# Kernel tuning notes

Hardware: AMD Instinct MI355X
Metric: run time of the kernel (lower is better)

Reference implementation:

```python
import jax, jax.numpy as jnp
import numpy as np

# Hard-coded video-latent geometry from the module's tile/untile rearranges
NT, NH, NW = 6, 6, 6          # tile grid
TT, TH, TW = 6, 8, 8          # tile sizes (6*8*8 = 384 tokens per tile)
TILE = TT * TH * TW           # 384
NTILES = NT * NH * NW         # 216
SEQ = NTILES * TILE           # 82944 = 36*48*48
# per-head sliding-tile windows (w_t, w_h, w_w), i.e. mask_strategy (sp_size=1)
WINDOWS = ((2, 1, 1), (1, 2, 2), (1, 1, 2), (1, 1, 1))


def tile(x):
    # 'b (t h w) head d' with (t,h,w)=(36,48,48) ->
    # 'b (n_t n_h n_w ts_t ts_h ts_w) head d'  (sp_size = 1)
    b, s, H, d = x.shape
    x = x.reshape(b, NT, TT, NH, TH, NW, TW, H, d)
    x = x.transpose(0, 1, 3, 5, 2, 4, 6, 7, 8)  # b, nt, nh, nw, tst, tsh, tsw, H, d
    return x.reshape(b, s, H, d)


def untile(x):
    b, s, H, d = x.shape
    x = x.reshape(b, NT, NH, NW, TT, TH, TW, H, d)
    x = x.transpose(0, 1, 4, 2, 5, 3, 6, 7, 8)  # b, nt, tst, nh, tsh, nw, tsw, H, d
    return x.reshape(b, s, H, d)


def _axis_window(w, n):
    # allowed key tile indices per query tile along one axis, clamped at borders
    q = jnp.arange(n)
    start = jnp.clip(q - (w - 1) // 2, 0, n - w)
    return start[:, None] + jnp.arange(w)[None, :]  # [n, w]


def _tile_gather_idx(wt, wh, ww):
    # flat key-tile ids [NTILES, wt*wh*ww] for every query tile
    it = _axis_window(wt, NT)  # [NT, wt]
    ih = _axis_window(wh, NH)  # [NH, wh]
    iw = _axis_window(ww, NW)  # [NW, ww]
    idx = (it[:, None, None, :, None, None] * (NH * NW)
           + ih[None, :, None, None, :, None] * NW
           + iw[None, None, :, None, None, :])
    return idx.reshape(NTILES, wt * wh * ww)


def sliding_tile_attention(q, k, v):
    # q, k, v: [B, S, H, d] in TILED order; returns [B, S, H, d] tiled order
    B, S, H, d = q.shape
    scale = 1.0 / jnp.sqrt(jnp.asarray(d, q.dtype))
    qt = q.reshape(B, NTILES, TILE, H, d)
    kt = k.reshape(B, NTILES, TILE, H, d)
    vt = v.reshape(B, NTILES, TILE, H, d)
    outs = []
    for h, (wt, wh, ww) in enumerate(WINDOWS):
        idx = _tile_gather_idx(wt, wh, ww)            # [NTILES, W]
        qh = qt[:, :, :, h, :]                        # [B, Q, 384, d]
        kg = kt[:, :, :, h, :][:, idx]                # [B, Q, W, 384, d]
        vg = vt[:, :, :, h, :][:, idx]
        W = idx.shape[1]
        kg = kg.reshape(B, NTILES, W * TILE, d)
        vg = vg.reshape(B, NTILES, W * TILE, d)
        s = jnp.einsum('bqnd,bqmd->bqnm', qh, kg) * scale
        p = jax.nn.softmax(s, axis=-1)
        outs.append(jnp.einsum('bqnm,bqmd->bqnd', p, vg))
    o = jnp.stack(outs, axis=3)                       # [B, Q, 384, H, d]
    return o.reshape(B, S, H, d)


def setup_inputs() -> dict:
    key = jax.random.key(0)
    kq, kk, kv = jax.random.split(key, 3)
    B, H, d = 1, 4, 64
    q = jax.random.normal(kq, (B, SEQ, H, d), dtype=jnp.float32)
    k = jax.random.normal(kk, (B, SEQ, H, d), dtype=jnp.float32)
    v = jax.random.normal(kv, (B, SEQ, H, d), dtype=jnp.float32)
    return {'q': q, 'k': k, 'v': v}


def reference(q, k, v):
    # parallel_attn_func, STA branch, sp_size = 1 (no sequence parallelism)
    qt_, kt_, vt_ = tile(q), tile(k), tile(v)
    x = sliding_tile_attention(qt_, kt_, vt_)
    return untile(x)
```

## Files before the change

### kernel.cpp

```cpp
#include <hip/hip_runtime.h>

typedef _Float16 half4 __attribute__((ext_vector_type(4)));
typedef _Float16 half8 __attribute__((ext_vector_type(8)));
typedef float    f32x4 __attribute__((ext_vector_type(4)));
typedef unsigned int u32x2 __attribute__((ext_vector_type(2)));
typedef unsigned int u32x4 __attribute__((ext_vector_type(4)));

__device__ __forceinline__ unsigned int pkrtz(float a, float b) {
    return __builtin_bit_cast(unsigned int, __builtin_amdgcn_cvt_pkrtz(a, b));
}
__device__ __forceinline__ half4 pack4(float a, float b, float c, float d) {
    u32x2 t; t[0] = pkrtz(a, b); t[1] = pkrtz(c, d);
    return __builtin_bit_cast(half4, t);
}
__device__ __forceinline__ half8 pack8(float a, float b, float c, float d,
                                       float e, float f, float gg, float h) {
    u32x4 t; t[0] = pkrtz(a, b); t[1] = pkrtz(c, d);
    t[2] = pkrtz(e, f); t[3] = pkrtz(gg, h);
    return __builtin_bit_cast(half8, t);
}
__device__ __forceinline__ float fexp2(float x) {
    return __builtin_amdgcn_exp2f(x);
}

#define ROWF 256
#define HDIM 64

__device__ __forceinline__ int intra_off(int j) {
    return 2304 * (j >> 6) + 48 * ((j >> 3) & 7) + (j & 7);
}

__device__ __forceinline__ int kperm32(int x) {
    return ((x & 4) << 2) | ((x & 24) >> 1) | (x & 3);
}

__global__ __launch_bounds__(512) void sta_kernel(
    const float* __restrict__ qg, const float* __restrict__ kg,
    const float* __restrict__ vg, float* __restrict__ out)
{
    __shared__ _Float16 Klds[128 * 64];
    __shared__ _Float16 Vlds[64 * 128];

    const int tid  = threadIdx.x;
    const int wave = tid >> 6;
    const int lane = tid & 63;
    const int g    = lane >> 4;
    const int c    = lane & 15;
    const int csw  = c >> 1;

    const int bid  = blockIdx.x;
    const int hidx = bid / 216;
    const int tile = bid - hidx * 216;
    const int head = (hidx == 0) ? 1 : (hidx == 1 ? 0 : hidx);

    const int nt = tile / 36;
    const int nh = (tile / 6) % 6;
    const int nw = tile % 6;
    const int tbase = 13824 * nt + 384 * nh + 8 * nw;

    int W, kb0; unsigned long long dpk;
    const int t0 = nt < 4 ? nt : 4;
    const int h0 = nh < 4 ? nh : 4;
    const int w0 = nw < 4 ? nw : 4;
    if (head == 0) {
        W = 2; kb0 = 13824 * t0 + 384 * nh + 8 * nw; dpk = (13824ULL << 16);
    } else if (head == 1) {
        W = 4; kb0 = 13824 * nt + 384 * h0 + 8 * w0;
        dpk = (8ULL << 16) | (384ULL << 32) | (392ULL << 48);
    } else if (head == 2) {
        W = 2; kb0 = 13824 * nt + 384 * nh + 8 * w0; dpk = (8ULL << 16);
    } else {
        W = 1; kb0 = tbase; dpk = 0ULL;
    }
    const int NC = W * 3;

    const float qscale = 0.125f * 1.44269504f;
    half8 qf[3][2];
    #pragma unroll
    for (int mt = 0; mt < 3; ++mt) {
        const int j = wave * 48 + mt * 16 + c;
        const float* qp = qg + (size_t)(tbase + intra_off(j)) * ROWF + head * HDIM;
        #pragma unroll
        for (int kc = 0; kc < 2; ++kc) {
            f32x4 a = *(const f32x4*)(qp + kc * 32 + g * 8);
            f32x4 b = *(const f32x4*)(qp + kc * 32 + g * 8 + 4);
            qf[mt][kc] = pack8(a[0] * qscale, a[1] * qscale, a[2] * qscale, a[3] * qscale,
                               b[0] * qscale, b[1] * qscale, b[2] * qscale, b[3] * qscale);
        }
    }

    f32x4 oacc[3][4];
    float m_r[3], l_r[3];
    #pragma unroll
    for (int mt = 0; mt < 3; ++mt) {
        #pragma unroll
        for (int dt = 0; dt < 4; ++dt) oacc[mt][dt] = (f32x4){0.f, 0.f, 0.f, 0.f};
        m_r[mt] = 8.0f;
        l_r[mt] = 0.f;
    }

    const int r4  = tid >> 4;
    const int sc4 = tid & 15;

    int toff0, toff1, toff2, toff3, krow0;
    {
        const int r0 = r4 * 4;
        toff0 = intra_off(r0 + 0);
        toff1 = intra_off(r0 + 1);
        toff2 = intra_off(r0 + 2);
        toff3 = intra_off(r0 + 3);
        krow0 = (r0 & 96) + kperm32(r0 & 31);
    }
    const size_t lin = (size_t)head * HDIM + sc4 * 4;

    f32x4 kr0, kr1, kr2, kr3, vr0, vr1, vr2, vr3;

#define ISSUE_N(N) do {                                                  \
        const int wi_ = (N) / 3;                                         \
        const int kb_ = kb0 + (int)((dpk >> (wi_ * 16)) & 0xFFFFULL)     \
                            + 4608 * ((N) - wi_ * 3);                    \
        const size_t a0 = (size_t)(kb_ + toff0) * ROWF + lin;            \
        const size_t a1 = (size_t)(kb_ + toff1) * ROWF + lin;            \
        const size_t a2 = (size_t)(kb_ + toff2) * ROWF + lin;            \
        const size_t a3 = (size_t)(kb_ + toff3) * ROWF + lin;            \
        kr0 = *(const f32x4*)(kg + a0); vr0 = *(const f32x4*)(vg + a0);  \
        kr1 = *(const f32x4*)(kg + a1); vr1 = *(const f32x4*)(vg + a1);  \
        kr2 = *(const f32x4*)(kg + a2); vr2 = *(const f32x4*)(vg + a2);  \
        kr3 = *(const f32x4*)(kg + a3); vr3 = *(const f32x4*)(vg + a3);  \
    } while (0)

#define COMMIT() do {                                                        \
        _Pragma("unroll")                                                    \
        for (int j = 0; j < 4; ++j) {                                        \
            const int kr_ = krow0 + j;                                       \
            const int ko_ = kr_ * 64 +                                       \
                (((sc4 >> 1) ^ ((kr_ >> 1) & 7)) << 3) + ((sc4 & 1) << 2);   \
            const f32x4 kv = (j == 0) ? kr0 : (j == 1) ? kr1                 \
                             : (j == 2) ? kr2 : kr3;                         \
            *(half4*)&Klds[ko_] = pack4(kv[0], kv[1], kv[2], kv[3]);         \
        }                                                                    \
        _Pragma("unroll")                                                    \
        for (int e = 0; e < 4; ++e) {                                        \
            const int vr_ = sc4 * 4 + e;                                     \
            const int vo_ = vr_ * 128 +                                      \
                (((r4 >> 1) ^ ((vr_ >> 1) & 7)) << 3) + ((r4 & 1) << 2);     \
            *(half4*)&Vlds[vo_] = pack4(vr0[e], vr1[e], vr2[e], vr3[e]);     \
        }                                                                    \
    } while (0)

    ISSUE_N(0);

    for (int ci = 0; ci < NC; ++ci) {
        COMMIT();
        __syncthreads();
        if (ci + 1 < NC) ISSUE_N(ci + 1);

        #pragma unroll
        for (int s = 0; s < 4; ++s) {
            f32x4 sacc[3][2];
            #pragma unroll
            for (int mt = 0; mt < 3; ++mt) {
                const float nm = -m_r[mt];
                sacc[mt][0] = (f32x4){nm, nm, nm, nm};
                sacc[mt][1] = (f32x4){nm, nm, nm, nm};
            }
            #pragma unroll
            for (int kc = 0; kc < 2; ++kc) {
                #pragma unroll
                for (int jt = 0; jt < 2; ++jt) {
                    const half8 kf = *(const half8*)
                        &Klds[(s * 32 + jt * 16 + c) * 64 + (((kc * 4 + g) ^ csw) << 3)];
                    #pragma unroll
                    for (int mt = 0; mt < 3; ++mt)
                        sacc[mt][jt] = __builtin_amdgcn_mfma_f32_16x16x32_f16(
                            kf, qf[mt][kc], sacc[mt][jt], 0, 0, 0);
                }
            }

            half8 pa[3];
            #pragma unroll
            for (int mt = 0; mt < 3; ++mt) {
                float p0 = fexp2(sacc[mt][0][0]), p1 = fexp2(sacc[mt][0][1]);
                float p2 = fexp2(sacc[mt][0][2]), p3 = fexp2(sacc[mt][0][3]);
                float p4 = fexp2(sacc[mt][1][0]), p5 = fexp2(sacc[mt][1][1]);
                float p6 = fexp2(sacc[mt][1][2]), p7 = fexp2(sacc[mt][1][3]);
                const float ma = fmaxf(fmaxf(fmaxf(sacc[mt][0][0], sacc[mt][0][1]),
                                             sacc[mt][0][2]), sacc[mt][0][3]);
                const float mb = fmaxf(fmaxf(fmaxf(sacc[mt][1][0], sacc[mt][1][1]),
                                             sacc[mt][1][2]), sacc[mt][1][3]);
                const float mm = fmaxf(ma, mb);

                if (__builtin_expect(!__all(mm <= 12.f), 0)) {
                    float mrow = mm;
                    mrow = fmaxf(mrow, __shfl_xor(mrow, 16, 64));
                    mrow = fmaxf(mrow, __shfl_xor(mrow, 32, 64));
                    const float delta = fmaxf(mrow, 0.f);
                    const float alpha = fexp2(-delta);
                    m_r[mt] += delta;
                    l_r[mt] *= alpha;
                    p0 *= alpha; p1 *= alpha; p2 *= alpha; p3 *= alpha;
                    p4 *= alpha; p5 *= alpha; p6 *= alpha; p7 *= alpha;
                    float ar[4];
                    #pragma unroll
                    for (int r = 0; r < 4; ++r) ar[r] = __shfl(alpha, g * 4 + r, 16);
                    #pragma unroll
                    for (int r = 0; r < 4; ++r)
                        #pragma unroll
                        for (int dt = 0; dt < 4; ++dt)
                            oacc[mt][dt][r] *= ar[r];
                }

                l_r[mt] += ((p0 + p1) + (p2 + p3)) + ((p4 + p5) + (p6 + p7));
                pa[mt] = pack8(p0, p1, p2, p3, p4, p5, p6, p7);
            }

            #pragma unroll
            for (int dt = 0; dt < 4; ++dt) {
                const half8 vb = *(const half8*)
                    &Vlds[(dt * 16 + c) * 128 + ((((s << 2) | g) ^ csw) << 3)];
                #pragma unroll
                for (int mt = 0; mt < 3; ++mt)
                    oacc[mt][dt] = __builtin_amdgcn_mfma_f32_16x16x32_f16(
                        pa[mt], vb, oacc[mt][dt], 0, 0, 0);
            }
        }
        __syncthreads();
    }
#undef ISSUE_N
#undef COMMIT

    #pragma unroll
    for (int mt = 0; mt < 3; ++mt) {
        float lf = l_r[mt];
        lf += __shfl_xor(lf, 16, 64);
        lf += __shfl_xor(lf, 32, 64);
        float lq[4];
        #pragma unroll
        for (int r = 0; r < 4; ++r) lq[r] = __shfl(lf, g * 4 + r, 16);
        #pragma unroll
        for (int r = 0; r < 4; ++r) {
            const int j = wave * 48 + mt * 16 + g * 4 + r;
            float* op = out + (size_t)(tbase + intra_off(j)) * ROWF + head * HDIM;
            const float linv = __builtin_amdgcn_rcpf(lq[r]);
            #pragma unroll
            for (int dt = 0; dt < 4; ++dt)
                op[dt * 16 + c] = oacc[mt][dt][r] * linv;
        }
    }
}

extern "C" void kernel_launch(void* const* d_in, const int* in_sizes, int n_in,
                              void* d_out, int out_size, void* d_ws, size_t ws_size,
                              hipStream_t stream) {
    const float* q = (const float*)d_in[0];
    const float* k = (const float*)d_in[1];
    const float* v = (const float*)d_in[2];
    float* o = (float*)d_out;
    dim3 grid(216 * 4);
    dim3 block(512);
    hipLaunchKernelGGL(sta_kernel, grid, block, 0, stream, q, k, v, o);
}
```

Baseline: 132.6 us.

## Compute softmax row sums via MFMA with ones and interleave heads per tile

```diff
diff --git a/kernel.cpp b/kernel.cpp
--- a/kernel.cpp
+++ b/kernel.cpp
@@ -49,9 +49,8 @@
     const int csw  = c >> 1;
 
     const int bid  = blockIdx.x;
-    const int hidx = bid / 216;
-    const int tile = bid - hidx * 216;
-    const int head = (hidx == 0) ? 1 : (hidx == 1 ? 0 : hidx);
+    const int tile = bid >> 2;
+    const int head = (bid + tile) & 3;
 
     const int nt = tile / 36;
     const int nh = (tile / 6) % 6;
@@ -89,14 +88,18 @@
         }
     }
 
+    u32x4 onep; onep[0] = onep[1] = onep[2] = onep[3] = 0x3C003C00u;
+    const half8 ones8 = __builtin_bit_cast(half8, onep);
+
     f32x4 oacc[3][4];
-    float m_r[3], l_r[3];
+    f32x4 lacc[3];
+    float m_r[3];
     #pragma unroll
     for (int mt = 0; mt < 3; ++mt) {
         #pragma unroll
         for (int dt = 0; dt < 4; ++dt) oacc[mt][dt] = (f32x4){0.f, 0.f, 0.f, 0.f};
+        lacc[mt] = (f32x4){0.f, 0.f, 0.f, 0.f};
         m_r[mt] = 8.0f;
-        l_r[mt] = 0.f;
     }
 
     const int r4  = tid >> 4;
@@ -184,10 +187,10 @@
                 float p2 = fexp2(sacc[mt][0][2]), p3 = fexp2(sacc[mt][0][3]);
                 float p4 = fexp2(sacc[mt][1][0]), p5 = fexp2(sacc[mt][1][1]);
                 float p6 = fexp2(sacc[mt][1][2]), p7 = fexp2(sacc[mt][1][3]);
-                const float ma = fmaxf(fmaxf(fmaxf(sacc[mt][0][0], sacc[mt][0][1]),
-                                             sacc[mt][0][2]), sacc[mt][0][3]);
-                const float mb = fmaxf(fmaxf(fmaxf(sacc[mt][1][0], sacc[mt][1][1]),
-                                             sacc[mt][1][2]), sacc[mt][1][3]);
+                const float ma = fmaxf(fmaxf(sacc[mt][0][0], sacc[mt][0][1]),
+                                       fmaxf(sacc[mt][0][2], sacc[mt][0][3]));
+                const float mb = fmaxf(fmaxf(sacc[mt][1][0], sacc[mt][1][1]),
+                                       fmaxf(sacc[mt][1][2], sacc[mt][1][3]));
                 const float mm = fmaxf(ma, mb);
 
                 if (__builtin_expect(!__all(mm <= 12.f), 0)) {
@@ -197,23 +200,27 @@
                     const float delta = fmaxf(mrow, 0.f);
                     const float alpha = fexp2(-delta);
                     m_r[mt] += delta;
-                    l_r[mt] *= alpha;
                     p0 *= alpha; p1 *= alpha; p2 *= alpha; p3 *= alpha;
                     p4 *= alpha; p5 *= alpha; p6 *= alpha; p7 *= alpha;
                     float ar[4];
                     #pragma unroll
                     for (int r = 0; r < 4; ++r) ar[r] = __shfl(alpha, g * 4 + r, 16);
                     #pragma unroll
-                    for (int r = 0; r < 4; ++r)
+                    for (int r = 0; r < 4; ++r) {
+                        lacc[mt][r] *= ar[r];
                         #pragma unroll
                         for (int dt = 0; dt < 4; ++dt)
                             oacc[mt][dt][r] *= ar[r];
+                    }
                 }
 
-                l_r[mt] += ((p0 + p1) + (p2 + p3)) + ((p4 + p5) + (p6 + p7));
                 pa[mt] = pack8(p0, p1, p2, p3, p4, p5, p6, p7);
             }
 
+            #pragma unroll
+            for (int mt = 0; mt < 3; ++mt)
+                lacc[mt] = __builtin_amdgcn_mfma_f32_16x16x32_f16(
+                    pa[mt], ones8, lacc[mt], 0, 0, 0);
             #pragma unroll
             for (int dt = 0; dt < 4; ++dt) {
                 const half8 vb = *(const half8*)
@@ -231,17 +238,11 @@
 
     #pragma unroll
     for (int mt = 0; mt < 3; ++mt) {
-        float lf = l_r[mt];
-        lf += __shfl_xor(lf, 16, 64);
-        lf += __shfl_xor(lf, 32, 64);
-        float lq[4];
-        #pragma unroll
-        for (int r = 0; r < 4; ++r) lq[r] = __shfl(lf, g * 4 + r, 16);
         #pragma unroll
         for (int r = 0; r < 4; ++r) {
             const int j = wave * 48 + mt * 16 + g * 4 + r;
             float* op = out + (size_t)(tbase + intra_off(j)) * ROWF + head * HDIM;
-            const float linv = __builtin_amdgcn_rcpf(lq[r]);
+            const float linv = __builtin_amdgcn_rcpf(lacc[mt][r]);
             #pragma unroll
             for (int dt = 0; dt < 4; ++dt)
                 op[dt * 16 + c] = oacc[mt][dt][r] * linv;
```

After: 212.1 us. 60.0% more time.

## Use persistent blocks with atomic work-stealing queue over tile-head items

Applied to the files above, without the earlier changes.

```diff
diff --git a/kernel.cpp b/kernel.cpp
--- a/kernel.cpp
+++ b/kernel.cpp
@@ -25,6 +25,7 @@
 
 #define ROWF 256
 #define HDIM 64
+#define NWORK 864
 
 __device__ __forceinline__ int intra_off(int j) {
     return 2304 * (j >> 6) + 48 * ((j >> 3) & 7) + (j & 7);
@@ -36,10 +37,12 @@
 
 __global__ __launch_bounds__(512) void sta_kernel(
     const float* __restrict__ qg, const float* __restrict__ kg,
-    const float* __restrict__ vg, float* __restrict__ out)
+    const float* __restrict__ vg, float* __restrict__ out,
+    int* __restrict__ wcnt)
 {
     __shared__ _Float16 Klds[128 * 64];
     __shared__ _Float16 Vlds[64 * 128];
+    __shared__ int s_w;
 
     const int tid  = threadIdx.x;
     const int wave = tid >> 6;
@@ -47,57 +50,6 @@
     const int g    = lane >> 4;
     const int c    = lane & 15;
     const int csw  = c >> 1;
-
-    const int bid  = blockIdx.x;
-    const int hidx = bid / 216;
-    const int tile = bid - hidx * 216;
-    const int head = (hidx == 0) ? 1 : (hidx == 1 ? 0 : hidx);
-
-    const int nt = tile / 36;
-    const int nh = (tile / 6) % 6;
-    const int nw = tile % 6;
-    const int tbase = 13824 * nt + 384 * nh + 8 * nw;
-
-    int W, kb0; unsigned long long dpk;
-    const int t0 = nt < 4 ? nt : 4;
-    const int h0 = nh < 4 ? nh : 4;
-    const int w0 = nw < 4 ? nw : 4;
-    if (head == 0) {
-        W = 2; kb0 = 13824 * t0 + 384 * nh + 8 * nw; dpk = (13824ULL << 16);
-    } else if (head == 1) {
-        W = 4; kb0 = 13824 * nt + 384 * h0 + 8 * w0;
-        dpk = (8ULL << 16) | (384ULL << 32) | (392ULL << 48);
-    } else if (head == 2) {
-        W = 2; kb0 = 13824 * nt + 384 * nh + 8 * w0; dpk = (8ULL << 16);
-    } else {
-        W = 1; kb0 = tbase; dpk = 0ULL;
-    }
-    const int NC = W * 3;
-
-    const float qscale = 0.125f * 1.44269504f;
-    half8 qf[3][2];
-    #pragma unroll
-    for (int mt = 0; mt < 3; ++mt) {
-        const int j = wave * 48 + mt * 16 + c;
-        const float* qp = qg + (size_t)(tbase + intra_off(j)) * ROWF + head * HDIM;
-        #pragma unroll
-        for (int kc = 0; kc < 2; ++kc) {
-            f32x4 a = *(const f32x4*)(qp + kc * 32 + g * 8);
-            f32x4 b = *(const f32x4*)(qp + kc * 32 + g * 8 + 4);
-            qf[mt][kc] = pack8(a[0] * qscale, a[1] * qscale, a[2] * qscale, a[3] * qscale,
-                               b[0] * qscale, b[1] * qscale, b[2] * qscale, b[3] * qscale);
-        }
-    }
-
-    f32x4 oacc[3][4];
-    float m_r[3], l_r[3];
-    #pragma unroll
-    for (int mt = 0; mt < 3; ++mt) {
-        #pragma unroll
-        for (int dt = 0; dt < 4; ++dt) oacc[mt][dt] = (f32x4){0.f, 0.f, 0.f, 0.f};
-        m_r[mt] = 8.0f;
-        l_r[mt] = 0.f;
-    }
 
     const int r4  = tid >> 4;
     const int sc4 = tid & 15;
@@ -111,9 +63,67 @@
         toff3 = intra_off(r0 + 3);
         krow0 = (r0 & 96) + kperm32(r0 & 31);
     }
-    const size_t lin = (size_t)head * HDIM + sc4 * 4;
+    const float qscale = 0.125f * 1.44269504f;
 
     f32x4 kr0, kr1, kr2, kr3, vr0, vr1, vr2, vr3;
+
+    for (;;) {
+        __syncthreads();
+        if (tid == 0) s_w = atomicAdd(wcnt, 1);
+        __syncthreads();
+        const int w = s_w;
+        if (w >= NWORK) return;
+
+        const int hidx = w / 216;
+        const int tile = w - hidx * 216;
+        const int head = (hidx == 0) ? 1 : (hidx == 1 ? 0 : hidx);
+
+        const int nt = tile / 36;
+        const int nh = (tile / 6) % 6;
+        const int nw = tile % 6;
+        const int tbase = 13824 * nt + 384 * nh + 8 * nw;
+
+        int W, kb0; unsigned long long dpk;
+        const int t0 = nt < 4 ? nt : 4;
+        const int h0 = nh < 4 ? nh : 4;
+        const int w0 = nw < 4 ? nw : 4;
+        if (head == 0) {
+            W = 2; kb0 = 13824 * t0 + 384 * nh + 8 * nw; dpk = (13824ULL << 16);
+        } else if (head == 1) {
+            W = 4; kb0 = 13824 * nt + 384 * h0 + 8 * w0;
+            dpk = (8ULL << 16) | (384ULL << 32) | (392ULL << 48);
+        } else if (head == 2) {
+            W = 2; kb0 = 13824 * nt + 384 * nh + 8 * w0; dpk = (8ULL << 16);
+        } else {
+            W = 1; kb0 = tbase; dpk = 0ULL;
+        }
+        const int NC = W * 3;
+
+        half8 qf[3][2];
+        #pragma unroll
+        for (int mt = 0; mt < 3; ++mt) {
+            const int j = wave * 48 + mt * 16 + c;
+            const float* qp = qg + (size_t)(tbase + intra_off(j)) * ROWF + head * HDIM;
+            #pragma unroll
+            for (int kc = 0; kc < 2; ++kc) {
+                f32x4 a = *(const f32x4*)(qp + kc * 32 + g * 8);
+                f32x4 b = *(const f32x4*)(qp + kc * 32 + g * 8 + 4);
+                qf[mt][kc] = pack8(a[0] * qscale, a[1] * qscale, a[2] * qscale, a[3] * qscale,
+                                   b[0] * qscale, b[1] * qscale, b[2] * qscale, b[3] * qscale);
+            }
+        }
+
+        f32x4 oacc[3][4];
+        float m_r[3], l_r[3];
+        #pragma unroll
+        for (int mt = 0; mt < 3; ++mt) {
+            #pragma unroll
+            for (int dt = 0; dt < 4; ++dt) oacc[mt][dt] = (f32x4){0.f, 0.f, 0.f, 0.f};
+            m_r[mt] = 8.0f;
+            l_r[mt] = 0.f;
+        }
+
+        const size_t lin = (size_t)head * HDIM + sc4 * 4;
 
 #define ISSUE_N(N) do {                                                  \
         const int wi_ = (N) / 3;                                         \
@@ -148,103 +158,104 @@
         }                                                                    \
     } while (0)
 
-    ISSUE_N(0);
-
-    for (int ci = 0; ci < NC; ++ci) {
-        COMMIT();
-        __syncthreads();
-        if (ci + 1 < NC) ISSUE_N(ci + 1);
-
-        #pragma unroll
-        for (int s = 0; s < 4; ++s) {
-            f32x4 sacc[3][2];
-            #pragma unroll
-            for (int mt = 0; mt < 3; ++mt) {
-                const float nm = -m_r[mt];
-                sacc[mt][0] = (f32x4){nm, nm, nm, nm};
-                sacc[mt][1] = (f32x4){nm, nm, nm, nm};
-            }
-            #pragma unroll
-            for (int kc = 0; kc < 2; ++kc) {
-                #pragma unroll
-                for (int jt = 0; jt < 2; ++jt) {
-                    const half8 kf = *(const half8*)
-                        &Klds[(s * 32 + jt * 16 + c) * 64 + (((kc * 4 + g) ^ csw) << 3)];
+        ISSUE_N(0);
+
+        for (int ci = 0; ci < NC; ++ci) {
+            COMMIT();
+            __syncthreads();
+            if (ci + 1 < NC) ISSUE_N(ci + 1);
+
+            #pragma unroll
+            for (int s = 0; s < 4; ++s) {
+                f32x4 sacc[3][2];
+                #pragma unroll
+                for (int mt = 0; mt < 3; ++mt) {
+                    const float nm = -m_r[mt];
+                    sacc[mt][0] = (f32x4){nm, nm, nm, nm};
+                    sacc[mt][1] = (f32x4){nm, nm, nm, nm};
+                }
+                #pragma unroll
+                for (int kc = 0; kc < 2; ++kc) {
+                    #pragma unroll
+                    for (int jt = 0; jt < 2; ++jt) {
+                        const half8 kf = *(const half8*)
+                            &Klds[(s * 32 + jt * 16 + c) * 64 + (((kc * 4 + g) ^ csw) << 3)];
+                        #pragma unroll
+                        for (int mt = 0; mt < 3; ++mt)
+                            sacc[mt][jt] = __builtin_amdgcn_mfma_f32_16x16x32_f16(
+                                kf, qf[mt][kc], sacc[mt][jt], 0, 0, 0);
+                    }
+                }
+
+                half8 pa[3];
+                #pragma unroll
+                for (int mt = 0; mt < 3; ++mt) {
+                    float p0 = fexp2(sacc[mt][0][0]), p1 = fexp2(sacc[mt][0][1]);
+                    float p2 = fexp2(sacc[mt][0][2]), p3 = fexp2(sacc[mt][0][3]);
+                    float p4 = fexp2(sacc[mt][1][0]), p5 = fexp2(sacc[mt][1][1]);
+                    float p6 = fexp2(sacc[mt][1][2]), p7 = fexp2(sacc[mt][1][3]);
+                    const float ma = fmaxf(fmaxf(sacc[mt][0][0], sacc[mt][0][1]),
+                                           fmaxf(sacc[mt][0][2], sacc[mt][0][3]));
+                    const float mb = fmaxf(fmaxf(sacc[mt][1][0], sacc[mt][1][1]),
+                                           fmaxf(sacc[mt][1][2], sacc[mt][1][3]));
+                    const float mm = fmaxf(ma, mb);
+
+                    if (__builtin_expect(!__all(mm <= 12.f), 0)) {
+                        float mrow = mm;
+                        mrow = fmaxf(mrow, __shfl_xor(mrow, 16, 64));
+                        mrow = fmaxf(mrow, __shfl_xor(mrow, 32, 64));
+                        const float delta = fmaxf(mrow, 0.f);
+                        const float alpha = fexp2(-delta);
+                        m_r[mt] += delta;
+                        l_r[mt] *= alpha;
+                        p0 *= alpha; p1 *= alpha; p2 *= alpha; p3 *= alpha;
+                        p4 *= alpha; p5 *= alpha; p6 *= alpha; p7 *= alpha;
+                        float ar[4];
+                        #pragma unroll
+                        for (int r = 0; r < 4; ++r) ar[r] = __shfl(alpha, g * 4 + r, 16);
+                        #pragma unroll
+                        for (int r = 0; r < 4; ++r)
+                            #pragma unroll
+                            for (int dt = 0; dt < 4; ++dt)
+                                oacc[mt][dt][r] *= ar[r];
+                    }
+
+                    l_r[mt] += ((p0 + p1) + (p2 + p3)) + ((p4 + p5) + (p6 + p7));
+                    pa[mt] = pack8(p0, p1, p2, p3, p4, p5, p6, p7);
+                }
+
+                #pragma unroll
+                for (int dt = 0; dt < 4; ++dt) {
+                    const half8 vb = *(const half8*)
+                        &Vlds[(dt * 16 + c) * 128 + ((((s << 2) | g) ^ csw) << 3)];
                     #pragma unroll
                     for (int mt = 0; mt < 3; ++mt)
-                        sacc[mt][jt] = __builtin_amdgcn_mfma_f32_16x16x32_f16(
-                            kf, qf[mt][kc], sacc[mt][jt], 0, 0, 0);
+                        oacc[mt][dt] = __builtin_amdgcn_mfma_f32_16x16x32_f16(
+                            pa[mt], vb, oacc[mt][dt], 0, 0, 0);
                 }
             }
-
-            half8 pa[3];
-            #pragma unroll
-            for (int mt = 0; mt < 3; ++mt) {
-                float p0 = fexp2(sacc[mt][0][0]), p1 = fexp2(sacc[mt][0][1]);
-                float p2 = fexp2(sacc[mt][0][2]), p3 = fexp2(sacc[mt][0][3]);
-                float p4 = fexp2(sacc[mt][1][0]), p5 = fexp2(sacc[mt][1][1]);
-                float p6 = fexp2(sacc[mt][1][2]), p7 = fexp2(sacc[mt][1][3]);
-                const float ma = fmaxf(fmaxf(fmaxf(sacc[mt][0][0], sacc[mt][0][1]),
-                                             sacc[mt][0][2]), sacc[mt][0][3]);
-                const float mb = fmaxf(fmaxf(fmaxf(sacc[mt][1][0], sacc[mt][1][1]),
-                                             sacc[mt][1][2]), sacc[mt][1][3]);
-                const float mm = fmaxf(ma, mb);
-
-                if (__builtin_expect(!__all(mm <= 12.f), 0)) {
-                    float mrow = mm;
-                    mrow = fmaxf(mrow, __shfl_xor(mrow, 16, 64));
-                    mrow = fmaxf(mrow, __shfl_xor(mrow, 32, 64));
-                    const float delta = fmaxf(mrow, 0.f);
-                    const float alpha = fexp2(-delta);
-                    m_r[mt] += delta;
-                    l_r[mt] *= alpha;
-                    p0 *= alpha; p1 *= alpha; p2 *= alpha; p3 *= alpha;
-                    p4 *= alpha; p5 *= alpha; p6 *= alpha; p7 *= alpha;
-                    float ar[4];
-                    #pragma unroll
-                    for (int r = 0; r < 4; ++r) ar[r] = __shfl(alpha, g * 4 + r, 16);
-                    #pragma unroll
-                    for (int r = 0; r < 4; ++r)
-                        #pragma unroll
-                        for (int dt = 0; dt < 4; ++dt)
-                            oacc[mt][dt][r] *= ar[r];
-                }
-
-                l_r[mt] += ((p0 + p1) + (p2 + p3)) + ((p4 + p5) + (p6 + p7));
-                pa[mt] = pack8(p0, p1, p2, p3, p4, p5, p6, p7);
-            }
-
-            #pragma unroll
-            for (int dt = 0; dt < 4; ++dt) {
-                const half8 vb = *(const half8*)
-                    &Vlds[(dt * 16 + c) * 128 + ((((s << 2) | g) ^ csw) << 3)];
-                #pragma unroll
-                for (int mt = 0; mt < 3; ++mt)
-                    oacc[mt][dt] = __builtin_amdgcn_mfma_f32_16x16x32_f16(
-                        pa[mt], vb, oacc[mt][dt], 0, 0, 0);
-            }
-        }
-        __syncthreads();
-    }
+            __syncthreads();
+        }
 #undef ISSUE_N
 #undef COMMIT
 
-    #pragma unroll
-    for (int mt = 0; mt < 3; ++mt) {
-        float lf = l_r[mt];
-        lf += __shfl_xor(lf, 16, 64);
-        lf += __shfl_xor(lf, 32, 64);
-        float lq[4];
         #pragma unroll
-        for (int r = 0; r < 4; ++r) lq[r] = __shfl(lf, g * 4 + r, 16);
-        #pragma unroll
-        for (int r = 0; r < 4; ++r) {
-            const int j = wave * 48 + mt * 16 + g * 4 + r;
-            float* op = out + (size_t)(tbase + intra_off(j)) * ROWF + head * HDIM;
-            const float linv = __builtin_amdgcn_rcpf(lq[r]);
-            #pragma unroll
-            for (int dt = 0; dt < 4; ++dt)
-                op[dt * 16 + c] = oacc[mt][dt][r] * linv;
+        for (int mt = 0; mt < 3; ++mt) {
+            float lf = l_r[mt];
+            lf += __shfl_xor(lf, 16, 64);
+            lf += __shfl_xor(lf, 32, 64);
+            float lq[4];
+            #pragma unroll
+            for (int r = 0; r < 4; ++r) lq[r] = __shfl(lf, g * 4 + r, 16);
+            #pragma unroll
+            for (int r = 0; r < 4; ++r) {
+                const int j = wave * 48 + mt * 16 + g * 4 + r;
+                float* op = out + (size_t)(tbase + intra_off(j)) * ROWF + head * HDIM;
+                const float linv = __builtin_amdgcn_rcpf(lq[r]);
+                #pragma unroll
+                for (int dt = 0; dt < 4; ++dt)
+                    op[dt * 16 + c] = oacc[mt][dt][r] * linv;
+            }
         }
     }
 }
@@ -256,7 +267,9 @@
     const float* k = (const float*)d_in[1];
     const float* v = (const float*)d_in[2];
     float* o = (float*)d_out;
-    dim3 grid(216 * 4);
+    int* wcnt = (int*)d_ws;
+    hipMemsetAsync(wcnt, 0, sizeof(int), stream);
+    dim3 grid(512);
     dim3 block(512);
-    hipLaunchKernelGGL(sta_kernel, grid, block, 0, stream, q, k, v, o);
-}
+    hipLaunchKernelGGL(sta_kernel, grid, block, 0, stream, q, k, v, o, wcnt);
+}
```

After: 137.2 us. +3.5%, slower.
